# Kernel tuning notes

Hardware: AMD Instinct MI355X
Metric: run time of the kernel (lower is better)

Reference implementation:

```python
import jax, jax.numpy as jnp
import numpy as np

B, N, D, OUT = 4, 2048, 128, 64
FWD_T, REV_T = 3, 3
NEG_BIG = 1e20  # matches tf source: GRAPH*1e20 - 1e20


def setup_inputs() -> dict:
    key = jax.random.key(0)
    k = jax.random.split(key, 9)
    INPUT = jax.random.normal(k[0], (B, N, D), dtype=jnp.float32)
    # binary adjacency with ~avg degree 64 (sparsity 64/N)
    CFG = (jax.random.uniform(k[1], (B, N, N)) < 64.0 / N).astype(jnp.float32)
    LFG = jnp.zeros((B, N, N), dtype=jnp.float32)  # unused by forward (commented out in source)
    s1 = 1.0 / np.sqrt(D)
    w1 = jax.random.uniform(k[2], (D, 1), minval=-s1, maxval=s1)
    b1 = jnp.zeros((1,), jnp.float32)
    w2 = jax.random.uniform(k[3], (D, 1), minval=-s1, maxval=s1)
    b2 = jnp.zeros((1,), jnp.float32)
    W = jax.random.uniform(k[4], (D, D), minval=-s1, maxval=s1)  # weightDense, no bias
    Wout = jax.random.uniform(k[5], (D, OUT), minval=-s1, maxval=s1)
    bout = jnp.zeros((OUT,), jnp.float32)
    return {"INPUT": INPUT, "CFG": CFG, "LFG": LFG, "w1": w1, "b1": b1,
            "w2": w2, "b2": b2, "W": W, "Wout": Wout, "bout": bout}


def _attention(x, g, w1, b1, w2, b2):
    # x: [B,N,D], g: [B,N,N] binary adjacency
    ah1 = x @ w1 + b1                      # [B,N,1]
    ah2 = x @ w2 + b2                      # [B,N,1]
    eij = ah1 + jnp.transpose(ah2, (0, 2, 1))   # [B,N,N]
    e_graph = g * NEG_BIG - NEG_BIG        # 0 where edge, -1e20 where no edge
    return jax.nn.softmax(jax.nn.leaky_relu(eij, negative_slope=0.2) + e_graph, axis=-1)


def _propagate(x, g, n_iter, w1, b1, w2, b2, W):
    for _ in range(n_iter):
        a = _attention(x, g, w1, b1, w2, b2) * g      # re-mask after softmax
        trans = jnp.einsum('bij,bjd->bid', a, x @ W)  # graph matmul (dropout off: eval mode)
        x = jax.nn.elu(x + trans)
    return x


def reference(INPUT, CFG, LFG, w1, b1, w2, b2, W, Wout, bout):
    fwd = _propagate(jax.nn.relu(INPUT), CFG, FWD_T, w1, b1, w2, b2, W)
    rev = _propagate(jax.nn.relu(INPUT), jnp.transpose(CFG, (0, 2, 1)), REV_T, w1, b1, w2, b2, W)
    mid = jnp.sum(fwd + rev, axis=1)       # [B,D]
    return mid @ Wout + bout               # [B,OUT]
```

## Files before the change

kernel.cpp:

```cpp
#include <hip/hip_runtime.h>
#include <hip/hip_fp16.h>
#include <cstdint>
#include <cstddef>

#define Bn 4
#define Nn 2048
#define Dn 128
#define OUTn 64
#define Sn 8
#define MAXDEG 128
#define NITER 3

typedef _Float16 half8 __attribute__((ext_vector_type(8)));
typedef float floatx4 __attribute__((ext_vector_type(4)));

__device__ __forceinline__ unsigned long long spread4(unsigned long long x) {
    x &= 0xFFFFull;
    x = (x | (x << 24)) & 0x000000FF000000FFull;
    x = (x | (x << 12)) & 0x000F000F000F000Full;
    x = (x | (x << 6))  & 0x0303030303030303ull;
    x = (x | (x << 3))  & 0x1111111111111111ull;
    return x;
}

__global__ void fwd_bits_init(const float4* __restrict__ cfg4,
                              unsigned long long* __restrict__ bits,
                              int* __restrict__ adj, int* __restrict__ deg,
                              const float4* __restrict__ in4,
                              __half* __restrict__ xh,
                              const float* __restrict__ W, __half* __restrict__ WhT,
                              const float* __restrict__ w1, const float* __restrict__ b1,
                              const float* __restrict__ w2, const float* __restrict__ b2,
                              float* __restrict__ ah1, float* __restrict__ ah2) {
    if (blockIdx.x >= (Bn * Nn) / 4 + (Bn * Nn) / 8) {
        int t = threadIdx.x;
        if (t < Dn) {
            for (int k = 0; k < Dn; ++k)
                WhT[(size_t)t * Dn + k] = __float2half(W[(size_t)k * Dn + t]);
        }
        return;
    }
    if (blockIdx.x >= (Bn * Nn) / 4) {
        int blk = blockIdx.x - (Bn * Nn) / 4;
        int t = threadIdx.x;
        int row = blk * 8 + (t >> 5);
        int q   = t & 31;
        float4 v = in4[(size_t)row * 32 + q];
        v.x = v.x > 0.f ? v.x : 0.f;
        v.y = v.y > 0.f ? v.y : 0.f;
        v.z = v.z > 0.f ? v.z : 0.f;
        v.w = v.w > 0.f ? v.w : 0.f;
        __half2 p0h = __floats2half2_rn(v.x, v.y);
        __half2 p1h = __floats2half2_rn(v.z, v.w);
        uint2 u2;
        u2.x = *(unsigned*)&p0h; u2.y = *(unsigned*)&p1h;
        ((uint2*)xh)[(size_t)row * 32 + q] = u2;
        ((uint2*)xh)[(size_t)(Bn * Nn) * 32 + (size_t)row * 32 + q] = u2;
        const float4* w14 = (const float4*)w1;
        const float4* w24 = (const float4*)w2;
        float4 wa = w14[q], wb = w24[q];
        float p1 = v.x * wa.x + v.y * wa.y + v.z * wa.z + v.w * wa.w;
        float p2 = v.x * wb.x + v.y * wb.y + v.z * wb.z + v.w * wb.w;
        #pragma unroll
        for (int o = 16; o >= 1; o >>= 1) {
            p1 += __shfl_xor(p1, o);
            p2 += __shfl_xor(p2, o);
        }
        if (q == 0) {
            float a1 = p1 + b1[0], a2 = p2 + b2[0];
            ah1[row] = a1; ah1[Bn * Nn + row] = a1;
            ah2[row] = a2; ah2[Bn * Nn + row] = a2;
        }
        return;
    }
    int row  = blockIdx.x * 4 + (threadIdx.x >> 6);
    int lane = threadIdx.x & 63;
    int b = row >> 11;
    int i = row & (Nn - 1);
    const float4* crow = cfg4 + (size_t)row * (Nn / 4);
    int* dst = adj + (size_t)row * MAXDEG;
    int cnt = 0;
    for (int j0 = 0; j0 < Nn; j0 += 256) {
        float4 v = crow[(j0 >> 2) + lane];
        int nib = (v.x != 0.f) | ((v.y != 0.f) << 1) |
                  ((v.z != 0.f) << 2) | ((v.w != 0.f) << 3);
        unsigned long long m0 = __ballot(nib & 1);
        unsigned long long m1 = __ballot(nib & 2);
        unsigned long long m2 = __ballot(nib & 4);
        unsigned long long m3 = __ballot(nib & 8);
        unsigned long long below = (1ull << lane) - 1ull;
        int off = __popcll(m0 & below) + __popcll(m1 & below) +
                  __popcll(m2 & below) + __popcll(m3 & below);
        int total = __popcll(m0) + __popcll(m1) + __popcll(m2) + __popcll(m3);
        int base = cnt + off;
        int col = j0 + 4 * lane;
        if (nib & 1) { if (base < MAXDEG) dst[base] = col;     base++; }
        if (nib & 2) { if (base < MAXDEG) dst[base] = col + 1; base++; }
        if (nib & 4) { if (base < MAXDEG) dst[base] = col + 2; base++; }
        if (nib & 8) { if (base < MAXDEG) dst[base] = col + 3; base++; }
        if (lane < 4) {
            int sh = lane << 4;
            unsigned long long w = spread4(m0 >> sh) | (spread4(m1 >> sh) << 1) |
                                   (spread4(m2 >> sh) << 2) | (spread4(m3 >> sh) << 3);
            int jw = (j0 >> 6) + lane;
            bits[((size_t)(b * 32 + jw)) * Nn + i] = w;
        }
        cnt += total;
    }
    if (lane == 0) deg[row] = (cnt < MAXDEG ? cnt : MAXDEG);
}

__device__ __forceinline__ void gemm_tile_mfma(const __half* __restrict__ xh,
                                               const __half* __restrict__ WhT,
                                               __half* __restrict__ xwh, int tile) {
    int lane = threadIdx.x & 63;
    int rowTile = tile >> 3, colTile = tile & 7;
    int mn = lane & 15, kseg = lane >> 4;
    const uint4* Arow = (const uint4*)(xh + ((size_t)(rowTile * 16 + mn)) * Dn);
    const uint4* Brow = (const uint4*)(WhT + ((size_t)(colTile * 16 + mn)) * Dn);
    floatx4 c = {0.f, 0.f, 0.f, 0.f};
    #pragma unroll
    for (int ks = 0; ks < 4; ++ks) {
        uint4 au = Arow[ks * 4 + kseg];
        uint4 bu = Brow[ks * 4 + kseg];
        half8 a = *(half8*)&au;
        half8 b = *(half8*)&bu;
        c = __builtin_amdgcn_mfma_f32_16x16x32_f16(a, b, c, 0, 0, 0);
    }
    int row = (lane >> 4) * 4;
    __half* dst = xwh + ((size_t)(rowTile * 16 + row)) * Dn + colTile * 16 + mn;
    #pragma unroll
    for (int rg = 0; rg < 4; ++rg)
        dst[(size_t)rg * Dn] = __float2half(c[rg]);
}

__global__ void gemm_rev(const __half* __restrict__ xh, const __half* __restrict__ WhT,
                         __half* __restrict__ xwh,
                         const unsigned long long* __restrict__ bits,
                         int* __restrict__ adj, int* __restrict__ deg) {
    if (blockIdx.x < 2048) {
        gemm_tile_mfma(xh, WhT, xwh, blockIdx.x * 4 + (threadIdx.x >> 6));
        return;
    }
    int r    = (blockIdx.x - 2048) * 4 + (threadIdx.x >> 6);
    int lane = threadIdx.x & 63;
    int b = r >> 11;
    int j = r & (Nn - 1);
    const unsigned long long* col = bits + ((size_t)(b * 32 + (j >> 6))) * Nn;
    int bit = j & 63;
    int out_r = (Bn + b) * Nn + j;
    int* dst = adj + (size_t)out_r * MAXDEG;
    int cnt = 0;
    for (int i0 = 0; i0 < Nn; i0 += 64) {
        unsigned long long word = col[i0 + lane];
        bool e = (word >> bit) & 1;
        unsigned long long m = __ballot(e);
        if (e) {
            int pos = cnt + __popcll(m & ((1ull << lane) - 1ull));
            if (pos < MAXDEG) dst[pos] = i0 + lane;
        }
        cnt += __popcll(m);
    }
    if (lane == 0) deg[out_r] = (cnt < MAXDEG ? cnt : MAXDEG);
}

__global__ void gemm_mfma(const __half* __restrict__ xh, const __half* __restrict__ WhT,
                          __half* __restrict__ xwh) {
    gemm_tile_mfma(xh, WhT, xwh, blockIdx.x * 4 + (threadIdx.x >> 6));
}

__global__ __launch_bounds__(256) void attn_agg(
        __half* __restrict__ xh,
        const __half* __restrict__ xwh,
        const int* __restrict__ adj, const int* __restrict__ deg,
        const float* __restrict__ ah1r, const float* __restrict__ ah2r,
        float* __restrict__ ah1w, float* __restrict__ ah2w,
        const float* __restrict__ gw1, const float* __restrict__ gb1,
        const float* __restrict__ gw2, const float* __restrict__ gb2) {
    int w    = threadIdx.x >> 6;
    int lane = threadIdx.x & 63;
    int s = blockIdx.x & 7;
    int i = (blockIdx.x >> 3) * 4 + w;
    int r = s * Nn + i;

    __shared__ float2 pn[4][MAXDEG];
    __shared__ float  aggF[4][Dn];

    int d = deg[r]; if (d > MAXDEG) d = MAXDEG;

    float a1 = ah1r[r];
    const int* al = adj + (size_t)r * MAXDEG;
    const float* ah2s = ah2r + (size_t)s * Nn;
    int jlo = 0, jhi = 0;
    float elo = -INFINITY, ehi = -INFINITY;
    if (lane < d) {
        jlo = al[lane];
        float e = a1 + ah2s[jlo];
        elo = e > 0.f ? e : 0.2f * e;
    }
    if (lane + 64 < d) {
        jhi = al[lane + 64];
        float e = a1 + ah2s[jhi];
        ehi = e > 0.f ? e : 0.2f * e;
    }
    float m = fmaxf(elo, ehi);
    #pragma unroll
    for (int o = 32; o > 0; o >>= 1) m = fmaxf(m, __shfl_xor(m, o));
    float exlo = (lane < d)      ? __expf(elo - m) : 0.f;
    float exhi = (lane + 64 < d) ? __expf(ehi - m) : 0.f;
    float sum = exlo + exhi;
    #pragma unroll
    for (int o = 32; o > 0; o >>= 1) sum += __shfl_xor(sum, o);
    float inv = (d > 0) ? 1.0f / sum : 0.f;

    pn[w][lane]      = make_float2(exlo, __int_as_float(jlo));
    pn[w][lane + 64] = make_float2(exhi, __int_as_float(jhi));

    const uint4* xwu = (const uint4*)(xwh + (size_t)s * Nn * Dn);
    int g = lane >> 4;
    int f = lane & 15;
    __half2 acc2[4];
    #pragma unroll
    for (int e = 0; e < 4; ++e) acc2[e] = __halves2half2(__float2half(0.f), __float2half(0.f));
    int dpad = (d + 15) & ~15;
    for (int base = 0; base < dpad; base += 16) {
        float2 q[4];
        uint4  v[4];
        #pragma unroll
        for (int t = 0; t < 4; ++t) q[t] = pn[w][base + 4 * t + g];
        #pragma unroll
        for (int t = 0; t < 4; ++t)
            v[t] = xwu[(size_t)__float_as_int(q[t].y) * 16 + f];
        #pragma unroll
        for (int t = 0; t < 4; ++t) {
            __half   ph = __float2half(q[t].x);
            __half2  p2 = __halves2half2(ph, ph);
            const __half2* hh = (const __half2*)&v[t];
            acc2[0] = __hfma2(p2, hh[0], acc2[0]);
            acc2[1] = __hfma2(p2, hh[1], acc2[1]);
            acc2[2] = __hfma2(p2, hh[2], acc2[2]);
            acc2[3] = __hfma2(p2, hh[3], acc2[3]);
        }
    }
    float2 f0 = __half22float2(acc2[0]);
    float2 f1 = __half22float2(acc2[1]);
    float2 f2 = __half22float2(acc2[2]);
    float2 f3 = __half22float2(acc2[3]);
    float accA[4] = { f0.x, f0.y, f1.x, f1.y };
    float accB[4] = { f2.x, f2.y, f3.x, f3.y };
    #pragma unroll
    for (int e = 0; e < 4; ++e) {
        accA[e] += __shfl_xor(accA[e], 16);
        accA[e] += __shfl_xor(accA[e], 32);
        accB[e] += __shfl_xor(accB[e], 16);
        accB[e] += __shfl_xor(accB[e], 32);
    }

    if (lane < 16) {
        #pragma unroll
        for (int e = 0; e < 4; ++e) {
            aggF[w][8 * lane + e]     = accA[e];
            aggF[w][8 * lane + 4 + e] = accB[e];
        }
    }

    float a0  = aggF[w][lane];
    float a1v = aggF[w][lane + 64];
    size_t xbase = (size_t)r * Dn;
    float v0 = __half2float(xh[xbase + lane]);
    float v1 = __half2float(xh[xbase + lane + 64]);
    float s0 = v0 + a0 * inv;
    float s1 = v1 + a1v * inv;
    s0 = s0 > 0.f ? s0 : (expf(s0) - 1.f);
    s1 = s1 > 0.f ? s1 : (expf(s1) - 1.f);
    xh[xbase + lane]      = __float2half(s0);
    xh[xbase + lane + 64] = __float2half(s1);

    float p1 = s0 * gw1[lane] + s1 * gw1[lane + 64];
    float p2 = s0 * gw2[lane] + s1 * gw2[lane + 64];
    #pragma unroll
    for (int o = 32; o > 0; o >>= 1) {
        p1 += __shfl_xor(p1, o);
        p2 += __shfl_xor(p2, o);
    }
    if (lane == 0) {
        ah1w[r] = p1 + gb1[0];
        ah2w[r] = p2 + gb2[0];
    }
}

__global__ void reduce_partial(const __half* __restrict__ xh, float* __restrict__ part) {
    int b = blockIdx.x >> 5;
    int c = blockIdx.x & 31;
    int tid = threadIdx.x;
    const __half* xf = xh + ((size_t)(b * Nn) + c * 64) * Dn;
    const __half* xr = xh + ((size_t)((4 + b) * Nn) + c * 64) * Dn;
    float sv = 0.f;
    for (int i = 0; i < 64; ++i)
        sv += __half2float(xf[(size_t)i * Dn + tid]) +
              __half2float(xr[(size_t)i * Dn + tid]);
    part[(size_t)blockIdx.x * Dn + tid] = sv;
}

__global__ void final_out(const float* __restrict__ part,
                          const float* __restrict__ Wout, const float* __restrict__ bout,
                          float* __restrict__ out) {
    int b = blockIdx.x;
    int tid = threadIdx.x;
    __shared__ float mid[Dn];
    float sv = 0.f;
    for (int c = 0; c < 32; ++c) sv += part[(size_t)(b * 32 + c) * Dn + tid];
    mid[tid] = sv;
    __syncthreads();
    if (tid < OUTn) {
        float o = bout[tid];
        #pragma unroll 4
        for (int k = 0; k < Dn; ++k) o = fmaf(mid[k], Wout[k * OUTn + tid], o);
        out[b * OUTn + tid] = o;
    }
}

extern "C" void kernel_launch(void* const* d_in, const int* in_sizes, int n_in,
                              void* d_out, int out_size, void* d_ws, size_t ws_size,
                              hipStream_t stream) {
    const float* INPUT = (const float*)d_in[0];
    const float* CFG   = (const float*)d_in[1];
    const float* w1    = (const float*)d_in[3];
    const float* b1    = (const float*)d_in[4];
    const float* w2    = (const float*)d_in[5];
    const float* b2    = (const float*)d_in[6];
    const float* Wm    = (const float*)d_in[7];
    const float* Wout  = (const float*)d_in[8];
    const float* bout  = (const float*)d_in[9];
    float* out = (float*)d_out;

    __half* xh   = (__half*)d_ws;
    __half* xwh  = xh + (size_t)Sn * Nn * Dn;
    __half* WhT  = xwh + (size_t)Sn * Nn * Dn;
    int*    adj  = (int*)(WhT + (size_t)Dn * Dn);
    int*    deg  = adj + (size_t)Sn * Nn * MAXDEG;
    float*  ah1a = (float*)(deg + Sn * Nn);
    float*  ah2a = ah1a + Sn * Nn;
    float*  ah1b = ah2a + Sn * Nn;
    float*  ah2b = ah1b + Sn * Nn;
    float*  part = ah2b + Sn * Nn;
    unsigned long long* bits = (unsigned long long*)(part + Bn * 32 * Dn);

    fwd_bits_init<<<(Bn * Nn) / 4 + (Bn * Nn) / 8 + 1, 256, 0, stream>>>(
        (const float4*)CFG, bits, adj, deg, (const float4*)INPUT,
        xh, Wm, WhT, w1, b1, w2, b2, ah1a, ah2a);

    for (int it = 0; it < NITER; ++it) {
        if (it == 0) {
            gemm_rev<<<4096, 256, 0, stream>>>(xh, WhT, xwh, bits, adj, deg);
        } else {
            gemm_mfma<<<2048, 256, 0, stream>>>(xh, WhT, xwh);
        }
        const float* r1 = (it & 1) ? ah1b : ah1a;
        const float* r2 = (it & 1) ? ah2b : ah2a;
        float* w1p = (it & 1) ? ah1a : ah1b;
        float* w2p = (it & 1) ? ah2a : ah2b;
        attn_agg<<<(Sn * Nn) / 4, 256, 0, stream>>>(
            xh, xwh, adj, deg, r1, r2, w1p, w2p, w1, b1, w2, b2);
    }

    reduce_partial<<<Bn * 32, 128, 0, stream>>>(xh, part);
    final_out     <<<Bn, 128, 0, stream>>>(part, Wout, bout, out);
}
```

Before: 133.1 us.

## Reassociate graph matmul: aggregate x first, then apply W via MFMA in-kernel

Instead of computing x@W for all nodes in a separate GEMM kernel and gathering from it, the attention kernel now gathers neighbour rows of x, normalises the aggregate, and multiplies the 4-row tile by W with MFMA inside the same kernel (padded to 16 rows in shared memory). This removes the per-iteration GEMM launch and its intermediate buffer write/read. The x buffer becomes double-buffered because neighbours must read the previous iteration's x. Reverse adjacency construction moves into its own kernel. The cost is that 12 of the 16 MFMA rows are zero padding, WhT is reloaded per block, and extra block-wide syncs are added.

After: 138.2 us. 3.8% more time.

```diff
diff --git a/kernel.cpp b/kernel.cpp
--- a/kernel.cpp
+++ b/kernel.cpp
@@ -10,6 +10,7 @@
 #define Sn 8
 #define MAXDEG 128
 #define NITER 3
+#define AS 136
 
 typedef _Float16 half8 __attribute__((ext_vector_type(8)));
 typedef float floatx4 __attribute__((ext_vector_type(4)));
@@ -110,39 +111,9 @@
     if (lane == 0) deg[row] = (cnt < MAXDEG ? cnt : MAXDEG);
 }
 
-__device__ __forceinline__ void gemm_tile_mfma(const __half* __restrict__ xh,
-                                               const __half* __restrict__ WhT,
-                                               __half* __restrict__ xwh, int tile) {
-    int lane = threadIdx.x & 63;
-    int rowTile = tile >> 3, colTile = tile & 7;
-    int mn = lane & 15, kseg = lane >> 4;
-    const uint4* Arow = (const uint4*)(xh + ((size_t)(rowTile * 16 + mn)) * Dn);
-    const uint4* Brow = (const uint4*)(WhT + ((size_t)(colTile * 16 + mn)) * Dn);
-    floatx4 c = {0.f, 0.f, 0.f, 0.f};
-    #pragma unroll
-    for (int ks = 0; ks < 4; ++ks) {
-        uint4 au = Arow[ks * 4 + kseg];
-        uint4 bu = Brow[ks * 4 + kseg];
-        half8 a = *(half8*)&au;
-        half8 b = *(half8*)&bu;
-        c = __builtin_amdgcn_mfma_f32_16x16x32_f16(a, b, c, 0, 0, 0);
-    }
-    int row = (lane >> 4) * 4;
-    __half* dst = xwh + ((size_t)(rowTile * 16 + row)) * Dn + colTile * 16 + mn;
-    #pragma unroll
-    for (int rg = 0; rg < 4; ++rg)
-        dst[(size_t)rg * Dn] = __float2half(c[rg]);
-}
-
-__global__ void gemm_rev(const __half* __restrict__ xh, const __half* __restrict__ WhT,
-                         __half* __restrict__ xwh,
-                         const unsigned long long* __restrict__ bits,
-                         int* __restrict__ adj, int* __restrict__ deg) {
-    if (blockIdx.x < 2048) {
-        gemm_tile_mfma(xh, WhT, xwh, blockIdx.x * 4 + (threadIdx.x >> 6));
-        return;
-    }
-    int r    = (blockIdx.x - 2048) * 4 + (threadIdx.x >> 6);
+__global__ void rev_adj(const unsigned long long* __restrict__ bits,
+                        int* __restrict__ adj, int* __restrict__ deg) {
+    int r    = blockIdx.x * 4 + (threadIdx.x >> 6);
     int lane = threadIdx.x & 63;
     int b = r >> 11;
     int j = r & (Nn - 1);
@@ -164,17 +135,12 @@
     if (lane == 0) deg[out_r] = (cnt < MAXDEG ? cnt : MAXDEG);
 }
 
-__global__ void gemm_mfma(const __half* __restrict__ xh, const __half* __restrict__ WhT,
-                          __half* __restrict__ xwh) {
-    gemm_tile_mfma(xh, WhT, xwh, blockIdx.x * 4 + (threadIdx.x >> 6));
-}
-
-__global__ __launch_bounds__(256) void attn_agg(
-        __half* __restrict__ xh,
-        const __half* __restrict__ xwh,
+__global__ __launch_bounds__(256) void attn_fused(
+        const __half* __restrict__ xh_r, __half* __restrict__ xh_w,
         const int* __restrict__ adj, const int* __restrict__ deg,
         const float* __restrict__ ah1r, const float* __restrict__ ah2r,
         float* __restrict__ ah1w, float* __restrict__ ah2w,
+        const __half* __restrict__ WhT,
         const float* __restrict__ gw1, const float* __restrict__ gb1,
         const float* __restrict__ gw2, const float* __restrict__ gb2) {
     int w    = threadIdx.x >> 6;
@@ -184,7 +150,14 @@
     int r = s * Nn + i;
 
     __shared__ float2 pn[4][MAXDEG];
-    __shared__ float  aggF[4][Dn];
+    __shared__ __half aggH[16 * AS];
+    __shared__ float  transF[4][Dn];
+
+    for (int idx = threadIdx.x; idx < 12 * (AS / 8); idx += 256) {
+        int zr = 4 + idx / (AS / 8);
+        int c8 = idx % (AS / 8);
+        ((uint4*)aggH)[zr * (AS / 8) + c8] = make_uint4(0, 0, 0, 0);
+    }
 
     int d = deg[r]; if (d > MAXDEG) d = MAXDEG;
 
@@ -216,7 +189,7 @@
     pn[w][lane]      = make_float2(exlo, __int_as_float(jlo));
     pn[w][lane + 64] = make_float2(exhi, __int_as_float(jhi));
 
-    const uint4* xwu = (const uint4*)(xwh + (size_t)s * Nn * Dn);
+    const uint4* xhu = (const uint4*)(xh_r + (size_t)s * Nn * Dn);
     int g = lane >> 4;
     int f = lane & 15;
     __half2 acc2[4];
@@ -230,7 +203,7 @@
         for (int t = 0; t < 4; ++t) q[t] = pn[w][base + 4 * t + g];
         #pragma unroll
         for (int t = 0; t < 4; ++t)
-            v[t] = xwu[(size_t)__float_as_int(q[t].y) * 16 + f];
+            v[t] = xhu[(size_t)__float_as_int(q[t].y) * 16 + f];
         #pragma unroll
         for (int t = 0; t < 4; ++t) {
             __half   ph = __float2half(q[t].x);
@@ -257,24 +230,52 @@
     }
 
     if (lane < 16) {
-        #pragma unroll
-        for (int e = 0; e < 4; ++e) {
-            aggF[w][8 * lane + e]     = accA[e];
-            aggF[w][8 * lane + 4 + e] = accB[e];
-        }
-    }
-
-    float a0  = aggF[w][lane];
-    float a1v = aggF[w][lane + 64];
+        __half2 h01 = __floats2half2_rn(accA[0] * inv, accA[1] * inv);
+        __half2 h23 = __floats2half2_rn(accA[2] * inv, accA[3] * inv);
+        __half2 h45 = __floats2half2_rn(accB[0] * inv, accB[1] * inv);
+        __half2 h67 = __floats2half2_rn(accB[2] * inv, accB[3] * inv);
+        uint4 u;
+        u.x = *(unsigned*)&h01; u.y = *(unsigned*)&h23;
+        u.z = *(unsigned*)&h45; u.w = *(unsigned*)&h67;
+        ((uint4*)aggH)[w * (AS / 8) + lane] = u;
+    }
+    __syncthreads();
+
+    {
+        int mn = lane & 15, kseg = lane >> 4;
+        #pragma unroll
+        for (int tt = 0; tt < 2; ++tt) {
+            int t = w + tt * 4;
+            const uint4* Brow = (const uint4*)(WhT + (size_t)(t * 16 + mn) * Dn);
+            floatx4 c = {0.f, 0.f, 0.f, 0.f};
+            #pragma unroll
+            for (int ks = 0; ks < 4; ++ks) {
+                uint4 au = ((const uint4*)aggH)[mn * (AS / 8) + ks * 4 + kseg];
+                uint4 bu = Brow[ks * 4 + kseg];
+                half8 a = *(half8*)&au;
+                half8 b = *(half8*)&bu;
+                c = __builtin_amdgcn_mfma_f32_16x16x32_f16(a, b, c, 0, 0, 0);
+            }
+            if (lane < 16) {
+                #pragma unroll
+                for (int rg = 0; rg < 4; ++rg)
+                    transF[rg][t * 16 + mn] = c[rg];
+            }
+        }
+    }
+    __syncthreads();
+
+    float a0  = transF[w][lane];
+    float a1v = transF[w][lane + 64];
     size_t xbase = (size_t)r * Dn;
-    float v0 = __half2float(xh[xbase + lane]);
-    float v1 = __half2float(xh[xbase + lane + 64]);
-    float s0 = v0 + a0 * inv;
-    float s1 = v1 + a1v * inv;
+    float v0 = __half2float(xh_r[xbase + lane]);
+    float v1 = __half2float(xh_r[xbase + lane + 64]);
+    float s0 = v0 + a0;
+    float s1 = v1 + a1v;
     s0 = s0 > 0.f ? s0 : (expf(s0) - 1.f);
     s1 = s1 > 0.f ? s1 : (expf(s1) - 1.f);
-    xh[xbase + lane]      = __float2half(s0);
-    xh[xbase + lane + 64] = __float2half(s1);
+    xh_w[xbase + lane]      = __float2half(s0);
+    xh_w[xbase + lane + 64] = __float2half(s1);
 
     float p1 = s0 * gw1[lane] + s1 * gw1[lane + 64];
     float p2 = s0 * gw2[lane] + s1 * gw2[lane + 64];
@@ -334,9 +335,9 @@
     const float* bout  = (const float*)d_in[9];
     float* out = (float*)d_out;
 
-    __half* xh   = (__half*)d_ws;
-    __half* xwh  = xh + (size_t)Sn * Nn * Dn;
-    __half* WhT  = xwh + (size_t)Sn * Nn * Dn;
+    __half* xh_a = (__half*)d_ws;
+    __half* xh_b = xh_a + (size_t)Sn * Nn * Dn;
+    __half* WhT  = xh_b + (size_t)Sn * Nn * Dn;
     int*    adj  = (int*)(WhT + (size_t)Dn * Dn);
     int*    deg  = adj + (size_t)Sn * Nn * MAXDEG;
     float*  ah1a = (float*)(deg + Sn * Nn);
@@ -348,22 +349,20 @@
 
     fwd_bits_init<<<(Bn * Nn) / 4 + (Bn * Nn) / 8 + 1, 256, 0, stream>>>(
         (const float4*)CFG, bits, adj, deg, (const float4*)INPUT,
-        xh, Wm, WhT, w1, b1, w2, b2, ah1a, ah2a);
+        xh_a, Wm, WhT, w1, b1, w2, b2, ah1a, ah2a);
+    rev_adj<<<(Bn * Nn) / 4, 256, 0, stream>>>(bits, adj, deg);
 
     for (int it = 0; it < NITER; ++it) {
-        if (it == 0) {
-            gemm_rev<<<4096, 256, 0, stream>>>(xh, WhT, xwh, bits, adj, deg);
-        } else {
-            gemm_mfma<<<2048, 256, 0, stream>>>(xh, WhT, xwh);
-        }
+        const __half* xr = (it & 1) ? xh_b : xh_a;
+        __half*       xw = (it & 1) ? xh_a : xh_b;
         const float* r1 = (it & 1) ? ah1b : ah1a;
         const float* r2 = (it & 1) ? ah2b : ah2a;
         float* w1p = (it & 1) ? ah1a : ah1b;
         float* w2p = (it & 1) ? ah2a : ah2b;
-        attn_agg<<<(Sn * Nn) / 4, 256, 0, stream>>>(
-            xh, xwh, adj, deg, r1, r2, w1p, w2p, w1, b1, w2, b2);
-    }
-
-    reduce_partial<<<Bn * 32, 128, 0, stream>>>(xh, part);
+        attn_fused<<<(Sn * Nn) / 4, 256, 0, stream>>>(
+            xr, xw, adj, deg, r1, r2, w1p, w2p, WhT, w1, b1, w2, b2);
+    }
+
+    reduce_partial<<<Bn * 32, 128, 0, stream>>>(xh_b, part);
     final_out     <<<Bn, 128, 0, stream>>>(part, Wout, bout, out);
 }
```
